# Performance work log

Hardware: AMD Instinct MI355X
Metric: run time of the kernel (lower is better)

## Reference

```python
import jax, jax.numpy as jnp
import numpy as np

D_MODEL = 1024
HEADS = 16
HEAD_DIM = D_MODEL // HEADS
FF = 4 * D_MODEL
EPS = 1e-5


def _layer_norm(x, g, b):
    mu = jnp.mean(x, axis=-1, keepdims=True)
    var = jnp.mean(jnp.square(x - mu), axis=-1, keepdims=True)
    return (x - mu) * jax.lax.rsqrt(var + EPS) * g + b


def setup_inputs() -> dict:
    key = jax.random.key(0)
    ks = jax.random.split(key, 12)
    s = 0.02
    inp = {
        "x": jax.random.normal(ks[0], (2, 2048, D_MODEL), dtype=jnp.float32),
        "Wq": jax.random.normal(ks[1], (D_MODEL, D_MODEL), dtype=jnp.float32) * s,
        "bq": jnp.zeros((D_MODEL,), jnp.float32),
        "Wk": jax.random.normal(ks[2], (D_MODEL, D_MODEL), dtype=jnp.float32) * s,
        "bk": jnp.zeros((D_MODEL,), jnp.float32),
        "Wv": jax.random.normal(ks[3], (D_MODEL, D_MODEL), dtype=jnp.float32) * s,
        "bv": jnp.zeros((D_MODEL,), jnp.float32),
        "Wm": jax.random.normal(ks[4], (D_MODEL, D_MODEL), dtype=jnp.float32) * s,
        "bm": jnp.zeros((D_MODEL,), jnp.float32),
        "W1": jax.random.normal(ks[5], (D_MODEL, FF), dtype=jnp.float32) * s,
        "b1": jnp.zeros((FF,), jnp.float32),
        "W2": jax.random.normal(ks[6], (FF, D_MODEL), dtype=jnp.float32) * s,
        "b2": jnp.zeros((D_MODEL,), jnp.float32),
        "g1": jnp.ones((D_MODEL,), jnp.float32),
        "be1": jnp.zeros((D_MODEL,), jnp.float32),
        "g2": jnp.ones((D_MODEL,), jnp.float32),
        "be2": jnp.zeros((D_MODEL,), jnp.float32),
    }
    return inp


def reference(x, Wq, bq, Wk, bk, Wv, bv, Wm, bm, W1, b1, W2, b2, g1, be1, g2, be2):
    B, L, _ = x.shape
    # self-attention: source = x, no pos, no masks
    q = (x @ Wq + bq).reshape(B, L, HEADS, HEAD_DIM).transpose(0, 2, 1, 3)
    k = (x @ Wk + bk).reshape(B, L, HEADS, HEAD_DIM).transpose(0, 2, 1, 3)
    v = (x @ Wv + bv).reshape(B, L, HEADS, HEAD_DIM).transpose(0, 2, 1, 3)
    scale = 1.0 / np.sqrt(HEAD_DIM).astype(np.float32)
    scores = jnp.einsum("bhld,bhsd->bhls", q, k) * scale  # [B,H,L,L]
    attn = jax.nn.softmax(scores, axis=-1)
    msg = jnp.einsum("bhls,bhsd->bhld", attn, v)
    msg = msg.transpose(0, 2, 1, 3).reshape(B, L, D_MODEL)
    msg = msg @ Wm + bm
    h = _layer_norm(x + msg, g1, be1)
    ffn = jax.nn.relu(h @ W1 + b1) @ W2 + b2
    return _layer_norm(h + ffn, g2, be2)
```

## Files before the change

### kernel.cpp

```cpp
#include <hip/hip_runtime.h>

#define D_MODEL 1024
#define N_TOK   4096
#define HEADS   16
#define FF_DIM  4096
#define SEQ_L   2048

typedef unsigned short u16;
typedef unsigned int   u32;
typedef __bf16 bf16x8 __attribute__((ext_vector_type(8)));
typedef float  f32x4  __attribute__((ext_vector_type(4)));

#define AS1C(p) ((const __attribute__((address_space(1))) void*)(p))
#define AS3(p)  ((__attribute__((address_space(3))) void*)(p))

__device__ __forceinline__ u16 f2bf(float f) {
    union { float f; unsigned u; } c; c.f = f;
    return (u16)((c.u + 0x7fffu + ((c.u >> 16) & 1u)) >> 16);
}
__device__ __forceinline__ float bf2f(u16 b) {
    union { unsigned u; float f; } c; c.u = ((unsigned)b) << 16;
    return c.f;
}
__device__ __forceinline__ u32 cvt_pk_bf16(float lo, float hi) {
    u32 r;
    asm("v_cvt_pk_bf16_f32 %0, %1, %2" : "=v"(r) : "v"(lo), "v"(hi));
    return r;
}

template<int RELU>
__global__ __launch_bounds__(512, 2)
void gemm_pipe(const u16* __restrict__ A, const u16* __restrict__ Bt,
               const float* __restrict__ bias, u16* __restrict__ C,
               int M, int N, int K)
{
    __shared__ u16 As[2][256 * 64];
    __shared__ u16 Bs[2][256 * 64];

    const int tid = threadIdx.x;
    const int wid = tid >> 6, lane = tid & 63;
    const int wr  = wid >> 2, wc = wid & 3;
    const int l15 = lane & 15, l16 = lane >> 4;
    const int r0  = blockIdx.y * 256, c0 = blockIdx.x * 256;

    const u16* Ab = A  + (size_t)r0 * K;
    const u16* Bb = Bt + (size_t)c0 * K;

    f32x4 acc[8][4];
#pragma unroll
    for (int m = 0; m < 8; ++m)
#pragma unroll
        for (int n = 0; n < 4; ++n) acc[m][n] = (f32x4){0.f, 0.f, 0.f, 0.f};

    auto stage = [&](u16* dst, const u16* src, int kbase) {
#pragma unroll
        for (int i = 0; i < 4; ++i) {
            const int r  = i * 64 + (tid >> 3);
            const int gc = (tid & 7) ^ (r & 7);
            __builtin_amdgcn_global_load_lds(AS1C(src + (size_t)r * K + kbase + gc * 8),
                                             AS3(dst + (i * 64 + (wid << 3)) * 64), 16, 0, 0);
        }
    };

    bf16x8 af[4][2], bbA[2][2], bbB[2][2];

    auto ldAf = [&](const u16* sl, int mh) {
#pragma unroll
        for (int m = 0; m < 4; ++m) {
            const int row = wr * 128 + (mh * 4 + m) * 16 + l15;
#pragma unroll
            for (int ks = 0; ks < 2; ++ks) {
                const int ch = (ks * 4 + l16) ^ (row & 7);
                af[m][ks] = *(const bf16x8*)&sl[row * 64 + ch * 8];
            }
        }
    };
    auto ldBf = [&](const u16* sl, int pair, bf16x8 (&bb)[2][2]) {
#pragma unroll
        for (int n = 0; n < 2; ++n) {
            const int row = wc * 64 + (pair * 2 + n) * 16 + l15;
#pragma unroll
            for (int ks = 0; ks < 2; ++ks) {
                const int ch = (ks * 4 + l16) ^ (row & 7);
                bb[n][ks] = *(const bf16x8*)&sl[row * 64 + ch * 8];
            }
        }
    };
    auto mm16 = [&](int mh, int pair, bf16x8 (&bb)[2][2]) {
        __builtin_amdgcn_s_setprio(1);
#pragma unroll
        for (int ks = 0; ks < 2; ++ks)
#pragma unroll
            for (int m = 0; m < 4; ++m)
#pragma unroll
                for (int n = 0; n < 2; ++n)
                    acc[mh * 4 + m][pair * 2 + n] =
                        __builtin_amdgcn_mfma_f32_16x16x32_bf16(af[m][ks], bb[n][ks],
                                                                acc[mh * 4 + m][pair * 2 + n], 0, 0, 0);
        __builtin_amdgcn_s_setprio(0);
    };

    const int nt = K >> 6;
    stage(&As[0][0], Ab, 0);
    stage(&Bs[0][0], Bb, 0);
    stage(&As[1][0], Ab, 64);

    for (int t = 0; t < nt; ++t) {
        u16* Asl = &As[t & 1][0];
        u16* Bsl = &Bs[t & 1][0];
        u16* Aso = &As[t & 1][0];
        u16* Bso = &Bs[(t + 1) & 1][0];

        if (t + 1 < nt) { asm volatile("s_waitcnt vmcnt(4)" ::: "memory"); }
        else            { asm volatile("s_waitcnt vmcnt(0)" ::: "memory"); }
        __builtin_amdgcn_s_barrier();
        ldAf(Asl, 0);
        ldBf(Bsl, 0, bbA);
        if (t + 1 < nt) stage(Bso, Bb, (t + 1) * 64);
        __builtin_amdgcn_s_barrier();
        mm16(0, 0, bbA);
        __builtin_amdgcn_s_barrier();
        ldBf(Bsl, 1, bbB);
        mm16(0, 1, bbB);
        __builtin_amdgcn_s_barrier();
        ldAf(Asl, 1);
        mm16(1, 0, bbA);
        __builtin_amdgcn_s_barrier();
        if (t + 2 < nt) stage(Aso, Ab, (t + 2) * 64);
        mm16(1, 1, bbB);
        __builtin_amdgcn_s_barrier();
    }

#pragma unroll
    for (int n = 0; n < 4; ++n) {
        const int col = c0 + wc * 64 + n * 16 + l15;
        const float bv = bias[col];
#pragma unroll
        for (int m = 0; m < 8; ++m) {
#pragma unroll
            for (int r = 0; r < 4; ++r) {
                const size_t row = (size_t)(r0 + wr * 128 + m * 16 + l16 * 4 + r);
                float v = acc[m][n][r] + bv;
                if (RELU) v = fmaxf(v, 0.f);
                C[row * N + col] = f2bf(v);
            }
        }
    }
}

template<int MFR, int RELU, int OUT_BF16>
__global__ __launch_bounds__(256)
void gemm_bt(const u16* __restrict__ A, const u16* __restrict__ Bt,
             const float* __restrict__ bias, void* __restrict__ Cv,
             int M, int N, int K)
{
    constexpr int BM = MFR * 32;
    __shared__ u16 As[BM * 64];
    __shared__ u16 Bs[128 * 64];

    const int tid  = threadIdx.x;
    const int wid  = tid >> 6, lane = tid & 63;
    const int wr   = wid >> 1, wc = wid & 1;
    const int l15  = lane & 15, l16 = lane >> 4;
    const int r0   = blockIdx.y * BM, c0 = blockIdx.x * 128;

    f32x4 acc[MFR][4];
#pragma unroll
    for (int m = 0; m < MFR; ++m)
#pragma unroll
        for (int n = 0; n < 4; ++n) acc[m][n] = (f32x4){0.f, 0.f, 0.f, 0.f};

    for (int k0 = 0; k0 < K; k0 += 64) {
        __syncthreads();
#pragma unroll
        for (int i = 0; i < BM / 32; ++i) {
            const int rb = wid * (BM / 4) + i * 8;
            const int r  = rb + (lane >> 3);
            const int gc = (lane & 7) ^ (r & 7);
            __builtin_amdgcn_global_load_lds(AS1C(A + (size_t)(r0 + r) * K + k0 + gc * 8),
                                             AS3(&As[rb * 64]), 16, 0, 0);
        }
#pragma unroll
        for (int i = 0; i < 4; ++i) {
            const int rb = wid * 32 + i * 8;
            const int r  = rb + (lane >> 3);
            const int gc = (lane & 7) ^ (r & 7);
            __builtin_amdgcn_global_load_lds(AS1C(Bt + (size_t)(c0 + r) * K + k0 + gc * 8),
                                             AS3(&Bs[rb * 64]), 16, 0, 0);
        }
        __syncthreads();
#pragma unroll
        for (int ks = 0; ks < 2; ++ks) {
            bf16x8 af[MFR], bb[4];
#pragma unroll
            for (int m = 0; m < MFR; ++m) {
                const int row = wr * (MFR * 16) + m * 16 + l15;
                const int ch  = (ks * 4 + l16) ^ (row & 7);
                af[m] = *(const bf16x8*)&As[row * 64 + ch * 8];
            }
#pragma unroll
            for (int n = 0; n < 4; ++n) {
                const int row = wc * 64 + n * 16 + l15;
                const int ch  = (ks * 4 + l16) ^ (row & 7);
                bb[n] = *(const bf16x8*)&Bs[row * 64 + ch * 8];
            }
#pragma unroll
            for (int m = 0; m < MFR; ++m)
#pragma unroll
                for (int n = 0; n < 4; ++n)
                    acc[m][n] = __builtin_amdgcn_mfma_f32_16x16x32_bf16(af[m], bb[n], acc[m][n], 0, 0, 0);
        }
    }

#pragma unroll
    for (int n = 0; n < 4; ++n) {
        const int col = c0 + wc * 64 + n * 16 + l15;
        const float bv = bias[col];
#pragma unroll
        for (int m = 0; m < MFR; ++m) {
#pragma unroll
            for (int r = 0; r < 4; ++r) {
                const size_t row = (size_t)(r0 + wr * (MFR * 16) + m * 16 + l16 * 4 + r);
                float v = acc[m][n][r] + bv;
                if (RELU) v = fmaxf(v, 0.f);
                if (OUT_BF16) ((u16*)Cv)[row * N + col] = f2bf(v);
                else          ((float*)Cv)[row * N + col] = v;
            }
        }
    }
}

__global__ __launch_bounds__(256)
void attn_mfma(const u16* __restrict__ qkv, u16* __restrict__ ao)
{
    __shared__ u16 Kl[64 * 64];
    __shared__ u32 Vt[64 * 32];

    const int tid = threadIdx.x;
    const int wid = tid >> 6, lane = tid & 63;
    const int l15 = lane & 15, l16 = lane >> 4;
    const int bh  = blockIdx.y, b = bh >> 4, h = bh & 15;
    const int ho  = h * 64;
    const size_t tb = (size_t)b * SEQ_L;
    const int q0  = blockIdx.x * 128;

    const u16* qg = qkv + (tb + q0) * 3072 + ho;
    const u16* kg = qkv + tb * 3072 + 1024 + ho;
    const u16* vg = qkv + tb * 3072 + 2048 + ho;

    const float SC = 0.18033688f;

    bf16x8 qa[2][2];
#pragma unroll
    for (int set = 0; set < 2; ++set)
#pragma unroll
        for (int ks = 0; ks < 2; ++ks) {
            union { bf16x8 v; u16 u[8]; u32 w[4]; } a, r;
            a.v = *(const bf16x8*)(qg + (size_t)(wid * 32 + set * 16 + l15) * 3072 + ks * 32 + l16 * 8);
#pragma unroll
            for (int e = 0; e < 4; ++e)
                r.w[e] = cvt_pk_bf16(bf2f(a.u[2 * e]) * SC, bf2f(a.u[2 * e + 1]) * SC);
            qa[set][ks] = r.v;
        }

    const int rp = lane & 31;
    const int vc = wid * 2 + (lane >> 5);

    f32x4 oacc[2][4];
#pragma unroll
    for (int set = 0; set < 2; ++set)
#pragma unroll
        for (int f = 0; f < 4; ++f) oacc[set][f] = (f32x4){0.f, 0.f, 0.f, 0.f};
    float m_c[2] = {-1e30f, -1e30f}, l_c[2] = {0.f, 0.f};

    for (int s0 = 0; s0 < SEQ_L; s0 += 64) {
        union { bf16x8 v; u16 u[8]; } ua, ub;
        ua.v = *(const bf16x8*)(vg + (size_t)(s0 + 2 * rp) * 3072 + vc * 8);
        ub.v = *(const bf16x8*)(vg + (size_t)(s0 + 2 * rp + 1) * 3072 + vc * 8);

        __syncthreads();
#pragma unroll
        for (int i = 0; i < 2; ++i) {
            const int rb = wid * 16 + i * 8;
            const int r  = rb + (lane >> 3);
            const int gc = (lane & 7) ^ (r & 7);
            __builtin_amdgcn_global_load_lds(AS1C(kg + (size_t)(s0 + r) * 3072 + gc * 8),
                                             AS3(&Kl[rb * 64]), 16, 0, 0);
        }
#pragma unroll
        for (int e = 0; e < 8; ++e) {
            const int d = vc * 8 + e;
            const int w = rp ^ (((d & 7) << 2) ^ ((d >> 3) << 1));
            Vt[d * 32 + w] = (u32)ua.u[e] | ((u32)ub.u[e] << 16);
        }
        __syncthreads();

        bf16x8 kb[4][2];
#pragma unroll
        for (int f = 0; f < 4; ++f)
#pragma unroll
            for (int ks = 0; ks < 2; ++ks) {
                const int row = f * 16 + l15;
                const int ch  = (ks * 4 + l16) ^ (row & 7);
                kb[f][ks] = *(const bf16x8*)&Kl[row * 64 + ch * 8];
            }

#pragma unroll
        for (int set = 0; set < 2; ++set) {
            f32x4 sacc[4];
#pragma unroll
            for (int f = 0; f < 4; ++f) sacc[f] = (f32x4){0.f, 0.f, 0.f, 0.f};
#pragma unroll
            for (int ks = 0; ks < 2; ++ks)
#pragma unroll
                for (int f = 0; f < 4; ++f)
                    sacc[f] = __builtin_amdgcn_mfma_f32_16x16x32_bf16(kb[f][ks], qa[set][ks], sacc[f], 0, 0, 0);

            float mx = sacc[0][0];
#pragma unroll
            for (int f = 0; f < 4; ++f)
#pragma unroll
                for (int r = 0; r < 4; ++r) mx = fmaxf(mx, sacc[f][r]);
            mx = fmaxf(mx, __shfl_xor(mx, 16));
            mx = fmaxf(mx, __shfl_xor(mx, 32));

            if (__any(mx > m_c[set] + 8.f)) {
                const float mnew = fmaxf(m_c[set], mx);
                const float corr = __builtin_exp2f(m_c[set] - mnew);
                m_c[set] = mnew;
                l_c[set] *= corr;
#pragma unroll
                for (int r = 0; r < 4; ++r) {
                    const float cr = __shfl(corr, l16 * 4 + r);
#pragma unroll
                    for (int f = 0; f < 4; ++f) oacc[set][f][r] *= cr;
                }
            }

            float rs = 0.f;
#pragma unroll
            for (int f = 0; f < 4; ++f)
#pragma unroll
                for (int r = 0; r < 4; ++r) {
                    const float p = __builtin_exp2f(sacc[f][r] - m_c[set]);
                    sacc[f][r] = p; rs += p;
                }
            rs += __shfl_xor(rs, 16);
            rs += __shfl_xor(rs, 32);
            l_c[set] += rs;

            u32 pk[4][2];
#pragma unroll
            for (int f = 0; f < 4; ++f) {
                pk[f][0] = cvt_pk_bf16(sacc[f][0], sacc[f][1]);
                pk[f][1] = cvt_pk_bf16(sacc[f][2], sacc[f][3]);
            }

#pragma unroll
            for (int S = 0; S < 2; ++S) {
                union { bf16x8 v; u32 u[4]; } af;
                af.u[0] = pk[2 * S][0];     af.u[1] = pk[2 * S][1];
                af.u[2] = pk[2 * S + 1][0]; af.u[3] = pk[2 * S + 1][1];
#pragma unroll
                for (int f2 = 0; f2 < 4; ++f2) {
                    const int d = f2 * 16 + l15;
                    const int swzd = ((d & 7) << 2) ^ ((d >> 3) << 1);
                    union { bf16x8 v; uint2 u[2]; } vb;
                    vb.u[0] = *(const uint2*)&Vt[d * 32 + ((16 * S + 2 * l16) ^ swzd)];
                    vb.u[1] = *(const uint2*)&Vt[d * 32 + ((16 * S + 8 + 2 * l16) ^ swzd)];
                    oacc[set][f2] = __builtin_amdgcn_mfma_f32_16x16x32_bf16(af.v, vb.v, oacc[set][f2], 0, 0, 0);
                }
            }
        }
    }

#pragma unroll
    for (int set = 0; set < 2; ++set)
#pragma unroll
        for (int r = 0; r < 4; ++r) {
            const float ld  = __shfl(l_c[set], l16 * 4 + r);
            const float inv = 1.f / ld;
            const size_t row = tb + q0 + wid * 32 + set * 16 + l16 * 4 + r;
#pragma unroll
            for (int f2 = 0; f2 < 4; ++f2)
                ao[row * 1024 + ho + f2 * 16 + l15] = f2bf(oacc[set][f2][r] * inv);
        }
}

template<int WB>
__global__ __launch_bounds__(256)
void add_ln(const float* __restrict__ x, const u16* __restrict__ y,
            const float* __restrict__ g, const float* __restrict__ be,
            float* __restrict__ outf, u16* __restrict__ outb)
{
    __shared__ float red[4];
    const int t = blockIdx.x, tid = threadIdx.x;
    const int c = tid * 4, lane = tid & 63, wv = tid >> 6;

    float4 a = *(const float4*)(x + (size_t)t * D_MODEL + c);
    ushort4 yb = *(const ushort4*)(y + (size_t)t * D_MODEL + c);
    float s[4] = {a.x + bf2f(yb.x), a.y + bf2f(yb.y), a.z + bf2f(yb.z), a.w + bf2f(yb.w)};

    float ps = s[0] + s[1] + s[2] + s[3];
#pragma unroll
    for (int off = 32; off > 0; off >>= 1) ps += __shfl_down(ps, off);
    if (lane == 0) red[wv] = ps;
    __syncthreads();
    const float mean = (red[0] + red[1] + red[2] + red[3]) * (1.f / D_MODEL);
    __syncthreads();

    float pv = 0.f;
#pragma unroll
    for (int u = 0; u < 4; ++u) { float d = s[u] - mean; pv += d * d; }
#pragma unroll
    for (int off = 32; off > 0; off >>= 1) pv += __shfl_down(pv, off);
    if (lane == 0) red[wv] = pv;
    __syncthreads();
    const float var = (red[0] + red[1] + red[2] + red[3]) * (1.f / D_MODEL);
    const float inv = rsqrtf(var + 1e-5f);

    float4 g4 = *(const float4*)(g + c);
    float4 b4 = *(const float4*)(be + c);
    float o[4];
#pragma unroll
    for (int u = 0; u < 4; ++u) o[u] = (s[u] - mean) * inv;
    float4 of = {o[0] * g4.x + b4.x, o[1] * g4.y + b4.y, o[2] * g4.z + b4.z, o[3] * g4.w + b4.w};
    *(float4*)(outf + (size_t)t * D_MODEL + c) = of;
    if (WB) {
        ushort4 ob = {f2bf(of.x), f2bf(of.y), f2bf(of.z), f2bf(of.w)};
        *(ushort4*)(outb + (size_t)t * D_MODEL + c) = ob;
    }
}

__global__ __launch_bounds__(256)
void prep(const float* __restrict__ Wq, const float* __restrict__ Wk,
          const float* __restrict__ Wv, const float* __restrict__ Wm,
          const float* __restrict__ W1, const float* __restrict__ W2,
          const float* __restrict__ x,
          const float* __restrict__ bq, const float* __restrict__ bk,
          const float* __restrict__ bv,
          u16* __restrict__ wqkv_t, u16* __restrict__ wm_t,
          u16* __restrict__ w1_t, u16* __restrict__ w2_t,
          u16* __restrict__ xb, float* __restrict__ bqkv)
{
    const int blk = blockIdx.x, tid = threadIdx.x;
    if (blk < 3072) {
        __shared__ float T[64][65];
        const float* src; u16* dst; int K, N, tile;
        if (blk < 256)       { src = Wq; dst = wqkv_t;               K = 1024; N = 1024; tile = blk; }
        else if (blk < 512)  { src = Wk; dst = wqkv_t + 1024 * 1024; K = 1024; N = 1024; tile = blk - 256; }
        else if (blk < 768)  { src = Wv; dst = wqkv_t + 2*1024*1024; K = 1024; N = 1024; tile = blk - 512; }
        else if (blk < 1024) { src = Wm; dst = wm_t;                 K = 1024; N = 1024; tile = blk - 768; }
        else if (blk < 2048) { src = W1; dst = w1_t;                 K = 1024; N = 4096; tile = blk - 1024; }
        else                 { src = W2; dst = w2_t;                 K = 4096; N = 1024; tile = blk - 2048; }
        const int ntn = N >> 6;
        const int n0 = (tile % ntn) * 64, k0 = (tile / ntn) * 64;
        const int rr = tid >> 4, cc = (tid & 15) * 4;
#pragma unroll
        for (int u = 0; u < 4; ++u) {
            const float4 v = *(const float4*)(src + (size_t)(k0 + rr + u * 16) * N + n0 + cc);
            T[rr + u * 16][cc + 0] = v.x; T[rr + u * 16][cc + 1] = v.y;
            T[rr + u * 16][cc + 2] = v.z; T[rr + u * 16][cc + 3] = v.w;
        }
        __syncthreads();
#pragma unroll
        for (int u = 0; u < 4; ++u) {
            const int n = rr + u * 16;
            ushort4 o;
            o.x = f2bf(T[cc + 0][n]); o.y = f2bf(T[cc + 1][n]);
            o.z = f2bf(T[cc + 2][n]); o.w = f2bf(T[cc + 3][n]);
            *(ushort4*)(dst + (size_t)(n0 + n) * K + k0 + cc) = o;
        }
    } else if (blk < 3072 + 4096) {
        const int i = (blk - 3072) * 1024 + tid * 4;
        float4 v = *(const float4*)(x + i);
        ushort4 o = {f2bf(v.x), f2bf(v.y), f2bf(v.z), f2bf(v.w)};
        *(ushort4*)(xb + i) = o;
    } else {
#pragma unroll
        for (int u = 0; u < 12; ++u) {
            const int i = u * 256 + tid;
            bqkv[i] = i < 1024 ? bq[i] : (i < 2048 ? bk[i - 1024] : bv[i - 2048]);
        }
    }
}

extern "C" void kernel_launch(void* const* d_in, const int* in_sizes, int n_in,
                              void* d_out, int out_size, void* d_ws, size_t ws_size,
                              hipStream_t stream)
{
    (void)in_sizes; (void)n_in; (void)out_size; (void)ws_size;

    const float* x   = (const float*)d_in[0];
    const float* Wq  = (const float*)d_in[1];
    const float* bq  = (const float*)d_in[2];
    const float* Wk  = (const float*)d_in[3];
    const float* bk  = (const float*)d_in[4];
    const float* Wv  = (const float*)d_in[5];
    const float* bv  = (const float*)d_in[6];
    const float* Wm  = (const float*)d_in[7];
    const float* bm  = (const float*)d_in[8];
    const float* W1  = (const float*)d_in[9];
    const float* b1  = (const float*)d_in[10];
    const float* W2  = (const float*)d_in[11];
    const float* b2  = (const float*)d_in[12];
    const float* g1  = (const float*)d_in[13];
    const float* be1 = (const float*)d_in[14];
    const float* g2  = (const float*)d_in[15];
    const float* be2 = (const float*)d_in[16];
    float* out = (float*)d_out;

    char* base = (char*)d_ws;
    const size_t MB = 1u << 20;
    u16*   wqkv_t = (u16*)(base);
    u16*   wm_t   = (u16*)(base + 6 * MB);
    u16*   w1_t   = (u16*)(base + 8 * MB);
    u16*   w2_t   = (u16*)(base + 16 * MB);
    float* bqkv   = (float*)(base + 24 * MB);
    u16*   xb     = (u16*)(base + 25 * MB);
    u16*   qkv    = (u16*)(base + 33 * MB);
    u16*   ao     = (u16*)(base + 57 * MB);
    u16*   f1     = (u16*)(base + 33 * MB);
    u16*   msg    = (u16*)(base + 25 * MB);
    u16*   ffn    = (u16*)(base + 25 * MB);
    float* hf     = (float*)(base + 65 * MB);
    u16*   hb     = (u16*)(base + 81 * MB);

    dim3 blk(256);
    prep<<<dim3(3072 + 4096 + 1), blk, 0, stream>>>(Wq, Wk, Wv, Wm, W1, W2, x,
                                                    bq, bk, bv,
                                                    wqkv_t, wm_t, w1_t, w2_t, xb, bqkv);

    gemm_pipe<0><<<dim3(12, 16), dim3(512), 0, stream>>>(xb, wqkv_t, bqkv, qkv, N_TOK, 3072, 1024);
    attn_mfma<<<dim3(SEQ_L / 128, 32), blk, 0, stream>>>(qkv, ao);
    gemm_bt<2, 0, 1><<<dim3(8, 64), blk, 0, stream>>>(ao, wm_t, bm, msg, N_TOK, 1024, 1024);
    add_ln<1><<<dim3(N_TOK), blk, 0, stream>>>(x, msg, g1, be1, hf, hb);
    gemm_pipe<1><<<dim3(16, 16), dim3(512), 0, stream>>>(hb, w1_t, b1, f1, N_TOK, FF_DIM, 1024);
    gemm_bt<2, 0, 1><<<dim3(8, 64), blk, 0, stream>>>(f1, w2_t, b2, ffn, N_TOK, 1024, FF_DIM);
    add_ln<0><<<dim3(N_TOK), blk, 0, stream>>>(hf, ffn, g2, be2, out, nullptr);
}
```

Measured before the change: 268.1 us.

## Add pipelined 128-tile GEMM, XCD block remap, and 8-wave attention

Replaces the unpipelined gemm_bt, used for the Wm and W2 projections, with a double-buffered 128x128 tile kernel that runs 512 threads, waits on vmcnt and raises MFMA priority with setprio. Both pipelined GEMMs now remap block IDs so that consecutive blocks are spread across the eight XCDs, aiming for better L2 locality. Attention now runs 8 waves of 16 query rows each instead of 4 waves of 32, which raises occupancy but has each K/V tile serve fewer query rows per wave. The row max now uses v_max3 instructions.

```diff
diff --git a/kernel.cpp b/kernel.cpp
--- a/kernel.cpp
+++ b/kernel.cpp
@@ -25,6 +25,11 @@
 __device__ __forceinline__ u32 cvt_pk_bf16(float lo, float hi) {
     u32 r;
     asm("v_cvt_pk_bf16_f32 %0, %1, %2" : "=v"(r) : "v"(lo), "v"(hi));
+    return r;
+}
+__device__ __forceinline__ float fmax3(float a, float b, float c) {
+    float r;
+    asm("v_max3_f32 %0, %1, %2, %3" : "=v"(r) : "v"(a), "v"(b), "v"(c));
     return r;
 }
 
@@ -41,7 +46,11 @@
     const int wid = tid >> 6, lane = tid & 63;
     const int wr  = wid >> 2, wc = wid & 3;
     const int l15 = lane & 15, l16 = lane >> 4;
-    const int r0  = blockIdx.y * 256, c0 = blockIdx.x * 256;
+
+    const int nwg = gridDim.x * gridDim.y;
+    int bid = blockIdx.y * gridDim.x + blockIdx.x;
+    bid = (bid & 7) * (nwg >> 3) + (bid >> 3);
+    const int r0 = (bid / gridDim.x) * 256, c0 = (bid % gridDim.x) * 256;
 
     const u16* Ab = A  + (size_t)r0 * K;
     const u16* Bb = Bt + (size_t)c0 * K;
@@ -148,89 +157,110 @@
     }
 }
 
-template<int MFR, int RELU, int OUT_BF16>
-__global__ __launch_bounds__(256)
-void gemm_bt(const u16* __restrict__ A, const u16* __restrict__ Bt,
-             const float* __restrict__ bias, void* __restrict__ Cv,
-             int M, int N, int K)
+template<int RELU>
+__global__ __launch_bounds__(512, 2)
+void gemm_pipe128(const u16* __restrict__ A, const u16* __restrict__ Bt,
+                  const float* __restrict__ bias, u16* __restrict__ C,
+                  int M, int N, int K)
 {
-    constexpr int BM = MFR * 32;
-    __shared__ u16 As[BM * 64];
-    __shared__ u16 Bs[128 * 64];
-
-    const int tid  = threadIdx.x;
-    const int wid  = tid >> 6, lane = tid & 63;
-    const int wr   = wid >> 1, wc = wid & 1;
-    const int l15  = lane & 15, l16 = lane >> 4;
-    const int r0   = blockIdx.y * BM, c0 = blockIdx.x * 128;
-
-    f32x4 acc[MFR][4];
-#pragma unroll
-    for (int m = 0; m < MFR; ++m)
-#pragma unroll
-        for (int n = 0; n < 4; ++n) acc[m][n] = (f32x4){0.f, 0.f, 0.f, 0.f};
-
-    for (int k0 = 0; k0 < K; k0 += 64) {
-        __syncthreads();
-#pragma unroll
-        for (int i = 0; i < BM / 32; ++i) {
-            const int rb = wid * (BM / 4) + i * 8;
-            const int r  = rb + (lane >> 3);
-            const int gc = (lane & 7) ^ (r & 7);
-            __builtin_amdgcn_global_load_lds(AS1C(A + (size_t)(r0 + r) * K + k0 + gc * 8),
-                                             AS3(&As[rb * 64]), 16, 0, 0);
-        }
-#pragma unroll
-        for (int i = 0; i < 4; ++i) {
-            const int rb = wid * 32 + i * 8;
-            const int r  = rb + (lane >> 3);
-            const int gc = (lane & 7) ^ (r & 7);
-            __builtin_amdgcn_global_load_lds(AS1C(Bt + (size_t)(c0 + r) * K + k0 + gc * 8),
-                                             AS3(&Bs[rb * 64]), 16, 0, 0);
-        }
-        __syncthreads();
-#pragma unroll
-        for (int ks = 0; ks < 2; ++ks) {
-            bf16x8 af[MFR], bb[4];
-#pragma unroll
-            for (int m = 0; m < MFR; ++m) {
-                const int row = wr * (MFR * 16) + m * 16 + l15;
-                const int ch  = (ks * 4 + l16) ^ (row & 7);
-                af[m] = *(const bf16x8*)&As[row * 64 + ch * 8];
-            }
-#pragma unroll
-            for (int n = 0; n < 4; ++n) {
-                const int row = wc * 64 + n * 16 + l15;
-                const int ch  = (ks * 4 + l16) ^ (row & 7);
-                bb[n] = *(const bf16x8*)&Bs[row * 64 + ch * 8];
-            }
-#pragma unroll
-            for (int m = 0; m < MFR; ++m)
-#pragma unroll
-                for (int n = 0; n < 4; ++n)
-                    acc[m][n] = __builtin_amdgcn_mfma_f32_16x16x32_bf16(af[m], bb[n], acc[m][n], 0, 0, 0);
-        }
-    }
-
-#pragma unroll
-    for (int n = 0; n < 4; ++n) {
-        const int col = c0 + wc * 64 + n * 16 + l15;
+    __shared__ u16 As[2][128 * 64];
+    __shared__ u16 Bs[2][128 * 64];
+
+    const int tid = threadIdx.x;
+    const int wid = tid >> 6, lane = tid & 63;
+    const int wr  = wid >> 2, wc = wid & 3;
+    const int l15 = lane & 15, l16 = lane >> 4;
+
+    const int nwg = gridDim.x * gridDim.y;
+    int bid = blockIdx.y * gridDim.x + blockIdx.x;
+    bid = (bid & 7) * (nwg >> 3) + (bid >> 3);
+    const int r0 = (bid / gridDim.x) * 128, c0 = (bid % gridDim.x) * 128;
+
+    const u16* Ab = A  + (size_t)r0 * K;
+    const u16* Bb = Bt + (size_t)c0 * K;
+
+    f32x4 acc[4][2];
+#pragma unroll
+    for (int m = 0; m < 4; ++m)
+#pragma unroll
+        for (int n = 0; n < 2; ++n) acc[m][n] = (f32x4){0.f, 0.f, 0.f, 0.f};
+
+    auto stage = [&](u16* dst, const u16* src, int kbase) {
+#pragma unroll
+        for (int i = 0; i < 2; ++i) {
+            const int r  = i * 64 + (tid >> 3);
+            const int gc = (tid & 7) ^ (r & 7);
+            __builtin_amdgcn_global_load_lds(AS1C(src + (size_t)r * K + kbase + gc * 8),
+                                             AS3(dst + (i * 64 + (wid << 3)) * 64), 16, 0, 0);
+        }
+    };
+
+    const int nt = K >> 6;
+    stage(&As[0][0], Ab, 0);  stage(&Bs[0][0], Bb, 0);
+    stage(&As[1][0], Ab, 64); stage(&Bs[1][0], Bb, 64);
+
+    for (int t = 0; t < nt; ++t) {
+        const u16* Asl = &As[t & 1][0];
+        const u16* Bsl = &Bs[t & 1][0];
+
+        if (t + 1 < nt) { asm volatile("s_waitcnt vmcnt(4)" ::: "memory"); }
+        else            { asm volatile("s_waitcnt vmcnt(0)" ::: "memory"); }
+        __builtin_amdgcn_s_barrier();
+
+        bf16x8 af[4][2], bb[2][2];
+#pragma unroll
+        for (int m = 0; m < 4; ++m) {
+            const int row = wr * 64 + m * 16 + l15;
+#pragma unroll
+            for (int ks = 0; ks < 2; ++ks) {
+                const int ch = (ks * 4 + l16) ^ (row & 7);
+                af[m][ks] = *(const bf16x8*)&Asl[row * 64 + ch * 8];
+            }
+        }
+#pragma unroll
+        for (int n = 0; n < 2; ++n) {
+            const int row = wc * 32 + n * 16 + l15;
+#pragma unroll
+            for (int ks = 0; ks < 2; ++ks) {
+                const int ch = (ks * 4 + l16) ^ (row & 7);
+                bb[n][ks] = *(const bf16x8*)&Bsl[row * 64 + ch * 8];
+            }
+        }
+        __builtin_amdgcn_s_setprio(1);
+#pragma unroll
+        for (int ks = 0; ks < 2; ++ks)
+#pragma unroll
+            for (int m = 0; m < 4; ++m)
+#pragma unroll
+                for (int n = 0; n < 2; ++n)
+                    acc[m][n] = __builtin_amdgcn_mfma_f32_16x16x32_bf16(af[m][ks], bb[n][ks], acc[m][n], 0, 0, 0);
+        __builtin_amdgcn_s_setprio(0);
+        __builtin_amdgcn_s_barrier();
+
+        if (t + 2 < nt) {
+            stage(&As[t & 1][0], Ab, (t + 2) * 64);
+            stage(&Bs[t & 1][0], Bb, (t + 2) * 64);
+        }
+    }
+
+#pragma unroll
+    for (int n = 0; n < 2; ++n) {
+        const int col = c0 + wc * 32 + n * 16 + l15;
         const float bv = bias[col];
 #pragma unroll
-        for (int m = 0; m < MFR; ++m) {
+        for (int m = 0; m < 4; ++m) {
 #pragma unroll
             for (int r = 0; r < 4; ++r) {
-                const size_t row = (size_t)(r0 + wr * (MFR * 16) + m * 16 + l16 * 4 + r);
+                const size_t row = (size_t)(r0 + wr * 64 + m * 16 + l16 * 4 + r);
                 float v = acc[m][n][r] + bv;
                 if (RELU) v = fmaxf(v, 0.f);
-                if (OUT_BF16) ((u16*)Cv)[row * N + col] = f2bf(v);
-                else          ((float*)Cv)[row * N + col] = v;
-            }
-        }
-    }
-}
-
-__global__ __launch_bounds__(256)
+                C[row * N + col] = f2bf(v);
+            }
+        }
+    }
+}
+
+__global__ __launch_bounds__(512, 4)
 void attn_mfma(const u16* __restrict__ qkv, u16* __restrict__ ao)
 {
     __shared__ u16 Kl[64 * 64];
@@ -250,141 +280,133 @@
 
     const float SC = 0.18033688f;
 
-    bf16x8 qa[2][2];
-#pragma unroll
-    for (int set = 0; set < 2; ++set)
-#pragma unroll
-        for (int ks = 0; ks < 2; ++ks) {
-            union { bf16x8 v; u16 u[8]; u32 w[4]; } a, r;
-            a.v = *(const bf16x8*)(qg + (size_t)(wid * 32 + set * 16 + l15) * 3072 + ks * 32 + l16 * 8);
-#pragma unroll
-            for (int e = 0; e < 4; ++e)
-                r.w[e] = cvt_pk_bf16(bf2f(a.u[2 * e]) * SC, bf2f(a.u[2 * e + 1]) * SC);
-            qa[set][ks] = r.v;
-        }
-
-    const int rp = lane & 31;
-    const int vc = wid * 2 + (lane >> 5);
-
-    f32x4 oacc[2][4];
-#pragma unroll
-    for (int set = 0; set < 2; ++set)
-#pragma unroll
-        for (int f = 0; f < 4; ++f) oacc[set][f] = (f32x4){0.f, 0.f, 0.f, 0.f};
-    float m_c[2] = {-1e30f, -1e30f}, l_c[2] = {0.f, 0.f};
+    bf16x8 qa[2];
+#pragma unroll
+    for (int ks = 0; ks < 2; ++ks) {
+        union { bf16x8 v; u16 u[8]; u32 w[4]; } a, r;
+        a.v = *(const bf16x8*)(qg + (size_t)(wid * 16 + l15) * 3072 + ks * 32 + l16 * 8);
+#pragma unroll
+        for (int e = 0; e < 4; ++e)
+            r.w[e] = cvt_pk_bf16(bf2f(a.u[2 * e]) * SC, bf2f(a.u[2 * e + 1]) * SC);
+        qa[ks] = r.v;
+    }
+
+    const int sp = tid & 31;
+    const int dc = tid >> 5;
+
+    f32x4 oacc[4];
+#pragma unroll
+    for (int f = 0; f < 4; ++f) oacc[f] = (f32x4){0.f, 0.f, 0.f, 0.f};
+    float m_c = -1e30f, l_c = 0.f;
 
     for (int s0 = 0; s0 < SEQ_L; s0 += 64) {
-        union { bf16x8 v; u16 u[8]; } ua, ub;
-        ua.v = *(const bf16x8*)(vg + (size_t)(s0 + 2 * rp) * 3072 + vc * 8);
-        ub.v = *(const bf16x8*)(vg + (size_t)(s0 + 2 * rp + 1) * 3072 + vc * 8);
+        ushort4 ua4 = *(const ushort4*)(vg + (size_t)(s0 + 2 * sp) * 3072 + dc * 4);
+        ushort4 ub4 = *(const ushort4*)(vg + (size_t)(s0 + 2 * sp + 1) * 3072 + dc * 4);
 
         __syncthreads();
-#pragma unroll
-        for (int i = 0; i < 2; ++i) {
-            const int rb = wid * 16 + i * 8;
-            const int r  = rb + (lane >> 3);
-            const int gc = (lane & 7) ^ (r & 7);
+        {
+            const int r  = tid >> 3;
+            const int gc = (tid & 7) ^ (r & 7);
             __builtin_amdgcn_global_load_lds(AS1C(kg + (size_t)(s0 + r) * 3072 + gc * 8),
-                                             AS3(&Kl[rb * 64]), 16, 0, 0);
-        }
-#pragma unroll
-        for (int e = 0; e < 8; ++e) {
-            const int d = vc * 8 + e;
-            const int w = rp ^ (((d & 7) << 2) ^ ((d >> 3) << 1));
-            Vt[d * 32 + w] = (u32)ua.u[e] | ((u32)ub.u[e] << 16);
+                                             AS3(&Kl[(wid * 8) * 64]), 16, 0, 0);
+        }
+        {
+            const u16* pu = (const u16*)&ua4;
+            const u16* pv = (const u16*)&ub4;
+#pragma unroll
+            for (int e = 0; e < 4; ++e) {
+                const int d = dc * 4 + e;
+                const int w = sp ^ (((d & 7) << 2) ^ ((d >> 3) << 1));
+                Vt[d * 32 + w] = (u32)pu[e] | ((u32)pv[e] << 16);
+            }
         }
         __syncthreads();
 
-        bf16x8 kb[4][2];
-#pragma unroll
-        for (int f = 0; f < 4; ++f)
-#pragma unroll
-            for (int ks = 0; ks < 2; ++ks) {
+        f32x4 sacc[4];
+#pragma unroll
+        for (int f = 0; f < 4; ++f) sacc[f] = (f32x4){0.f, 0.f, 0.f, 0.f};
+#pragma unroll
+        for (int ks = 0; ks < 2; ++ks)
+#pragma unroll
+            for (int f = 0; f < 4; ++f) {
                 const int row = f * 16 + l15;
                 const int ch  = (ks * 4 + l16) ^ (row & 7);
-                kb[f][ks] = *(const bf16x8*)&Kl[row * 64 + ch * 8];
-            }
-
-#pragma unroll
-        for (int set = 0; set < 2; ++set) {
-            f32x4 sacc[4];
-#pragma unroll
-            for (int f = 0; f < 4; ++f) sacc[f] = (f32x4){0.f, 0.f, 0.f, 0.f};
-#pragma unroll
-            for (int ks = 0; ks < 2; ++ks)
-#pragma unroll
-                for (int f = 0; f < 4; ++f)
-                    sacc[f] = __builtin_amdgcn_mfma_f32_16x16x32_bf16(kb[f][ks], qa[set][ks], sacc[f], 0, 0, 0);
-
-            float mx = sacc[0][0];
-#pragma unroll
-            for (int f = 0; f < 4; ++f)
-#pragma unroll
-                for (int r = 0; r < 4; ++r) mx = fmaxf(mx, sacc[f][r]);
-            mx = fmaxf(mx, __shfl_xor(mx, 16));
-            mx = fmaxf(mx, __shfl_xor(mx, 32));
-
-            if (__any(mx > m_c[set] + 8.f)) {
-                const float mnew = fmaxf(m_c[set], mx);
-                const float corr = __builtin_exp2f(m_c[set] - mnew);
-                m_c[set] = mnew;
-                l_c[set] *= corr;
-#pragma unroll
-                for (int r = 0; r < 4; ++r) {
-                    const float cr = __shfl(corr, l16 * 4 + r);
-#pragma unroll
-                    for (int f = 0; f < 4; ++f) oacc[set][f][r] *= cr;
-                }
-            }
-
-            float rs = 0.f;
-#pragma unroll
-            for (int f = 0; f < 4; ++f)
-#pragma unroll
-                for (int r = 0; r < 4; ++r) {
-                    const float p = __builtin_exp2f(sacc[f][r] - m_c[set]);
-                    sacc[f][r] = p; rs += p;
-                }
-            rs += __shfl_xor(rs, 16);
-            rs += __shfl_xor(rs, 32);
-            l_c[set] += rs;
-
-            u32 pk[4][2];
-#pragma unroll
-            for (int f = 0; f < 4; ++f) {
-                pk[f][0] = cvt_pk_bf16(sacc[f][0], sacc[f][1]);
-                pk[f][1] = cvt_pk_bf16(sacc[f][2], sacc[f][3]);
-            }
-
-#pragma unroll
-            for (int S = 0; S < 2; ++S) {
-                union { bf16x8 v; u32 u[4]; } af;
-                af.u[0] = pk[2 * S][0];     af.u[1] = pk[2 * S][1];
-                af.u[2] = pk[2 * S + 1][0]; af.u[3] = pk[2 * S + 1][1];
-#pragma unroll
-                for (int f2 = 0; f2 < 4; ++f2) {
-                    const int d = f2 * 16 + l15;
-                    const int swzd = ((d & 7) << 2) ^ ((d >> 3) << 1);
-                    union { bf16x8 v; uint2 u[2]; } vb;
-                    vb.u[0] = *(const uint2*)&Vt[d * 32 + ((16 * S + 2 * l16) ^ swzd)];
-                    vb.u[1] = *(const uint2*)&Vt[d * 32 + ((16 * S + 8 + 2 * l16) ^ swzd)];
-                    oacc[set][f2] = __builtin_amdgcn_mfma_f32_16x16x32_bf16(af.v, vb.v, oacc[set][f2], 0, 0, 0);
-                }
-            }
-        }
-    }
-
-#pragma unroll
-    for (int set = 0; set < 2; ++set)
-#pragma unroll
-        for (int r = 0; r < 4; ++r) {
-            const float ld  = __shfl(l_c[set], l16 * 4 + r);
-            const float inv = 1.f / ld;
-            const size_t row = tb + q0 + wid * 32 + set * 16 + l16 * 4 + r;
-#pragma unroll
-            for (int f2 = 0; f2 < 4; ++f2)
-                ao[row * 1024 + ho + f2 * 16 + l15] = f2bf(oacc[set][f2][r] * inv);
-        }
+                bf16x8 kb = *(const bf16x8*)&Kl[row * 64 + ch * 8];
+                sacc[f] = __builtin_amdgcn_mfma_f32_16x16x32_bf16(kb, qa[ks], sacc[f], 0, 0, 0);
+            }
+
+        float mx;
+        {
+            float a0 = fmax3(sacc[0][0], sacc[0][1], sacc[0][2]);
+            float a1 = fmax3(sacc[0][3], sacc[1][0], sacc[1][1]);
+            float a2 = fmax3(sacc[1][2], sacc[1][3], sacc[2][0]);
+            float a3 = fmax3(sacc[2][1], sacc[2][2], sacc[2][3]);
+            float a4 = fmax3(sacc[3][0], sacc[3][1], sacc[3][2]);
+            float b0 = fmax3(a0, a1, sacc[3][3]);
+            float b1 = fmax3(a2, a3, a4);
+            mx = fmaxf(b0, b1);
+        }
+        mx = fmaxf(mx, __shfl_xor(mx, 16));
+        mx = fmaxf(mx, __shfl_xor(mx, 32));
+
+        if (__any(mx > m_c + 8.f)) {
+            const float mnew = fmaxf(m_c, mx);
+            const float corr = __builtin_exp2f(m_c - mnew);
+            m_c = mnew;
+            l_c *= corr;
+#pragma unroll
+            for (int r = 0; r < 4; ++r) {
+                const float cr = __shfl(corr, l16 * 4 + r);
+#pragma unroll
+                for (int f = 0; f < 4; ++f) oacc[f][r] *= cr;
+            }
+        }
+
+        float rs = 0.f;
+#pragma unroll
+        for (int f = 0; f < 4; ++f)
+#pragma unroll
+            for (int r = 0; r < 4; ++r) {
+                const float p = __builtin_exp2f(sacc[f][r] - m_c);
+                sacc[f][r] = p; rs += p;
+            }
+        rs += __shfl_xor(rs, 16);
+        rs += __shfl_xor(rs, 32);
+        l_c += rs;
+
+        u32 pk[4][2];
+#pragma unroll
+        for (int f = 0; f < 4; ++f) {
+            pk[f][0] = cvt_pk_bf16(sacc[f][0], sacc[f][1]);
+            pk[f][1] = cvt_pk_bf16(sacc[f][2], sacc[f][3]);
+        }
+
+#pragma unroll
+        for (int S = 0; S < 2; ++S) {
+            union { bf16x8 v; u32 u[4]; } af;
+            af.u[0] = pk[2 * S][0];     af.u[1] = pk[2 * S][1];
+            af.u[2] = pk[2 * S + 1][0]; af.u[3] = pk[2 * S + 1][1];
+#pragma unroll
+            for (int f2 = 0; f2 < 4; ++f2) {
+                const int d = f2 * 16 + l15;
+                const int swzd = ((d & 7) << 2) ^ ((d >> 3) << 1);
+                union { bf16x8 v; uint2 u[2]; } vb;
+                vb.u[0] = *(const uint2*)&Vt[d * 32 + ((16 * S + 2 * l16) ^ swzd)];
+                vb.u[1] = *(const uint2*)&Vt[d * 32 + ((16 * S + 8 + 2 * l16) ^ swzd)];
+                oacc[f2] = __builtin_amdgcn_mfma_f32_16x16x32_bf16(af.v, vb.v, oacc[f2], 0, 0, 0);
+            }
+        }
+    }
+
+#pragma unroll
+    for (int r = 0; r < 4; ++r) {
+        const float ld  = __shfl(l_c, l16 * 4 + r);
+        const float inv = 1.f / ld;
+        const size_t row = tb + q0 + wid * 16 + l16 * 4 + r;
+#pragma unroll
+        for (int f2 = 0; f2 < 4; ++f2)
+            ao[row * 1024 + ho + f2 * 16 + l15] = f2bf(oacc[f2][r] * inv);
+    }
 }
 
 template<int WB>
@@ -532,10 +554,10 @@
                                                     wqkv_t, wm_t, w1_t, w2_t, xb, bqkv);
 
     gemm_pipe<0><<<dim3(12, 16), dim3(512), 0, stream>>>(xb, wqkv_t, bqkv, qkv, N_TOK, 3072, 1024);
-    attn_mfma<<<dim3(SEQ_L / 128, 32), blk, 0, stream>>>(qkv, ao);
-    gemm_bt<2, 0, 1><<<dim3(8, 64), blk, 0, stream>>>(ao, wm_t, bm, msg, N_TOK, 1024, 1024);
+    attn_mfma<<<dim3(SEQ_L / 128, 32), dim3(512), 0, stream>>>(qkv, ao);
+    gemm_pipe128<0><<<dim3(8, 32), dim3(512), 0, stream>>>(ao, wm_t, bm, msg, N_TOK, 1024, 1024);
     add_ln<1><<<dim3(N_TOK), blk, 0, stream>>>(x, msg, g1, be1, hf, hb);
     gemm_pipe<1><<<dim3(16, 16), dim3(512), 0, stream>>>(hb, w1_t, b1, f1, N_TOK, FF_DIM, 1024);
-    gemm_bt<2, 0, 1><<<dim3(8, 64), blk, 0, stream>>>(f1, w2_t, b2, ffn, N_TOK, 1024, FF_DIM);
+    gemm_pipe128<0><<<dim3(8, 32), dim3(512), 0, stream>>>(f1, w2_t, b2, ffn, N_TOK, 1024, FF_DIM);
     add_ln<0><<<dim3(N_TOK), blk, 0, stream>>>(hf, ffn, g2, be2, out, nullptr);
 }
```

New measurement: 258.0 us. 3.7% less time.
